# Kernel optimization log

Measured on AMD Instinct MI355X. Metric: run time of the kernel, lower is better.

Reference implementation:

```python
import jax, jax.numpy as jnp
import numpy as np

N = 4096        # batch size (rows)
K = 4           # instances per class -> num_instances in the torch code
D = 256         # embedding dim
MARGIN = 0.5
SAMPLE_KEY = jax.random.key(42)  # fixed key: deterministic stand-in for torch.multinomial


def setup_inputs() -> dict:
    key = jax.random.key(0)
    x = jax.random.normal(key, (N, D), dtype=jnp.float32)
    # L2-normalize like typical metric-learning embeddings so sims are in [-1, 1]
    inputs = x / jnp.linalg.norm(x, axis=1, keepdims=True)
    targets = (jnp.arange(N) // K).astype(jnp.int32)  # P*K batch: equal-size classes
    return {"inputs": inputs, "targets": targets}


def reference(inputs, targets):
    n = inputs.shape[0]
    km1 = K - 1                 # positives per row
    n_neg = n - K               # negatives per row

    sim = inputs @ inputs.T                                   # [n, n]
    same = targets[:, None] == targets[None, :]
    eye = jnp.eye(n, dtype=bool)
    pos_mask = same & ~eye
    neg_mask = ~same

    # masked_select + per-row sort: masked entries -> +inf, ascending sort,
    # keep first count entries (counts are uniform across rows)
    pos_sorted = jnp.sort(jnp.where(pos_mask, sim, jnp.inf), axis=1)[:, :km1]   # [n, K-1]
    neg_sorted = jnp.sort(jnp.where(neg_mask, sim, jnp.inf), axis=1)[:, :n_neg] # [n, n-K]

    pos_d = jnp.mean(pos_sorted)
    neg_d = jnp.mean(neg_sorted)

    # GaussDistribution per row over negatives
    neg_mean = jnp.mean(neg_sorted, axis=1, keepdims=True)
    neg_std = jnp.sqrt(jnp.mean((neg_sorted - neg_mean) ** 2, axis=1, keepdims=True))
    # NOTE: the original uses exp(+(x-mu)^2 / (2 sigma^2)) (no minus sign) -- faithful
    logprob = (neg_sorted - neg_mean) ** 2 / (2.0 * neg_std ** 2)               # [n, n-K]

    # multinomial without replacement ~ Gumbel top-k on log-weights
    gumbel = -jnp.log(-jnp.log(
        jax.random.uniform(SAMPLE_KEY, logprob.shape, minval=1e-20, maxval=1.0)))
    _, neg_idx = jax.lax.top_k(logprob + gumbel, km1)                            # [n, K-1]
    neg_pair = jnp.take_along_axis(neg_sorted, neg_idx, axis=1)                  # [n, K-1]

    pos_loss = jnp.mean(jnp.log1p(jnp.exp(-2.0 * (pos_sorted - MARGIN))), axis=1)
    neg_loss = 0.04 * jnp.mean(jnp.log1p(jnp.exp(50.0 * (neg_pair - MARGIN))), axis=1)
    loss = jnp.sum(pos_loss + neg_loss) / n

    # prec: fraction of rows where hardest positive > hardest sampled negative + 0.05
    c = jnp.sum(pos_sorted[:, -1] > jnp.max(neg_pair, axis=1) + 0.05)
    prec = c.astype(jnp.float32) / n

    return loss, prec, pos_d, neg_d
```

## Files before the change

kernel.cpp:

```cpp
#include <hip/hip_runtime.h>
#include <hip/hip_bf16.h>
#include <cstdint>
#include <cfloat>
#include <math.h>

#define NN 4096
#define DD 256
#define NNEG 4092
#define MARGIN 0.5f
#define NB 4096

__device__ __forceinline__ uint32_t rotl32(uint32_t x, int r) {
  return (x << r) | (x >> (32 - r));
}

__device__ __forceinline__ void threefry2x32_42(uint32_t x0, uint32_t x1,
                                                uint32_t& o0, uint32_t& o1) {
  const uint32_t k0 = 0u, k1 = 42u;
  const uint32_t k2 = k0 ^ k1 ^ 0x1BD11BDAu;
  x0 += k0; x1 += k1;
#define TF_R(r) { x0 += x1; x1 = rotl32(x1, r); x1 ^= x0; }
  TF_R(13) TF_R(15) TF_R(26) TF_R(6)
  x0 += k1; x1 += k2 + 1u;
  TF_R(17) TF_R(29) TF_R(16) TF_R(24)
  x0 += k2; x1 += k0 + 2u;
  TF_R(13) TF_R(15) TF_R(26) TF_R(6)
  x0 += k0; x1 += k1 + 3u;
  TF_R(17) TF_R(29) TF_R(16) TF_R(24)
  x0 += k1; x1 += k2 + 4u;
  TF_R(13) TF_R(15) TF_R(26) TF_R(6)
  x0 += k2; x1 += k0 + 5u;
#undef TF_R
  o0 = x0; o1 = x1;
}

__device__ __forceinline__ float gumbel_at(uint32_t f) {
  uint32_t o0, o1;
  threefry2x32_42(0u, f, o0, o1);
  uint32_t bits = o0 ^ o1;
  uint32_t fb = (bits >> 9) | 0x3F800000u;
  float fl = __uint_as_float(fb) - 1.0f;
  float u = fmaxf(1e-20f, fl + 1e-20f);
  return -logf(-logf(u));
}

__device__ __forceinline__ int bucket_of(float v) {
  return (int)fminf(fmaxf((v + 0.5f) * (float)NB, 0.0f), (float)(NB - 1));
}

#define BT 128
#define NT (NN / BT)
#define BK 64
#define LDSS 68

__global__ __launch_bounds__(256) void gemm_sim(const float* __restrict__ X,
                                                float* __restrict__ S) {
  __shared__ float As[BT * LDSS];
  __shared__ float Bs[BT * LDSS];
  const int tid = threadIdx.x;
  const int tx = tid & 15, ty = tid >> 4;

  int b = blockIdx.x, bi = 0;
  while (b >= NT - bi) { b -= NT - bi; bi++; }
  const int bj = bi + b;
  const int rowBase = bi * BT, colBase = bj * BT;

  float acc[8][8] = {};
  for (int kb = 0; kb < DD; kb += BK) {
#pragma unroll
    for (int it = 0; it < 8; ++it) {
      int idx = tid + 256 * it;
      int r = idx >> 4, c4 = idx & 15;
      float4 av = *(const float4*)(X + (size_t)(rowBase + r) * DD + kb + c4 * 4);
      float4 bv = *(const float4*)(X + (size_t)(colBase + r) * DD + kb + c4 * 4);
      *(float4*)(As + r * LDSS + c4 * 4) = av;
      *(float4*)(Bs + r * LDSS + c4 * 4) = bv;
    }
    __syncthreads();
    for (int k = 0; k < BK; k += 4) {
      float4 a[8], bfr[8];
#pragma unroll
      for (int i = 0; i < 8; ++i) a[i] = *(const float4*)(As + (ty + 16 * i) * LDSS + k);
#pragma unroll
      for (int j = 0; j < 8; ++j) bfr[j] = *(const float4*)(Bs + (tx + 16 * j) * LDSS + k);
#pragma unroll
      for (int i = 0; i < 8; ++i)
#pragma unroll
        for (int j = 0; j < 8; ++j) {
          acc[i][j] += a[i].x * bfr[j].x;
          acc[i][j] += a[i].y * bfr[j].y;
          acc[i][j] += a[i].z * bfr[j].z;
          acc[i][j] += a[i].w * bfr[j].w;
        }
    }
    __syncthreads();
  }
#pragma unroll
  for (int i = 0; i < 8; ++i)
#pragma unroll
    for (int j = 0; j < 8; ++j)
      S[(size_t)(rowBase + ty + 16 * i) * NN + colBase + tx + 16 * j] = acc[i][j];
  if (bi != bj) {
#pragma unroll
    for (int i = 0; i < 8; ++i)
#pragma unroll
      for (int j = 0; j < 8; ++j)
        S[(size_t)(colBase + tx + 16 * j) * NN + rowBase + ty + 16 * i] = acc[i][j];
  }
}

__global__ __launch_bounds__(256) void row_kernel(const float* __restrict__ S,
                                                  float* __restrict__ acc) {
  __shared__ uint32_t hist[NB];
  __shared__ uint32_t offs[NB];
  __shared__ float sval[NN];
  __shared__ float sh[24];
  __shared__ uint32_t wtot[4];

  const int row = blockIdx.x;
  const int tid = threadIdx.x;
  const int lane = tid & 63, wid = tid >> 6;

#pragma unroll
  for (int it = 0; it < 4; ++it)
    ((uint4*)hist)[tid + 256 * it] = make_uint4(0u, 0u, 0u, 0u);

  const float4* src = (const float4*)(S + (size_t)row * NN);
  const int pslot = row >> 2;
  float vv[16];
#pragma unroll
  for (int it = 0; it < 4; ++it) {
    int slot = tid + 256 * it;
    float4 t4 = src[slot];
    if (slot == pslot) {
      sh[16] = t4.x; sh[17] = t4.y; sh[18] = t4.z; sh[19] = t4.w;
      t4.x = INFINITY; t4.y = INFINITY; t4.z = INFINITY; t4.w = INFINITY;
    }
    vv[4 * it + 0] = t4.x; vv[4 * it + 1] = t4.y;
    vv[4 * it + 2] = t4.z; vv[4 * it + 3] = t4.w;
  }

  float s = 0.0f;
#pragma unroll
  for (int e = 0; e < 16; ++e) if (vv[e] < 1e30f) s += vv[e];
#pragma unroll
  for (int off = 32; off > 0; off >>= 1) s += __shfl_down(s, off, 64);
  if (lane == 0) sh[5 + wid] = s;
  __syncthreads();

#pragma unroll
  for (int e = 0; e < 16; ++e) atomicAdd(&hist[bucket_of(vv[e])], 1u);

  if (tid == 0) {
    int self = row & 3;
    float p[3]; int m = 0;
#pragma unroll
    for (int c = 0; c < 4; ++c)
      if (c != self) p[m++] = sh[16 + c];
    float t;
    if (p[0] > p[1]) { t = p[0]; p[0] = p[1]; p[1] = t; }
    if (p[1] > p[2]) { t = p[1]; p[1] = p[2]; p[2] = t; }
    if (p[0] > p[1]) { t = p[0]; p[0] = p[1]; p[1] = t; }
    sh[0] = p[0]; sh[1] = p[1]; sh[2] = p[2];
    float tot = sh[5] + sh[6] + sh[7] + sh[8];
    sh[9] = tot;
    sh[3] = tot / (float)NNEG;
  }
  __syncthreads();

  uint32_t h[16];
  uint32_t s16 = 0;
#pragma unroll
  for (int jj = 0; jj < 4; ++jj) {
    uint4 h4 = ((const uint4*)hist)[tid * 4 + jj];
    h[4 * jj + 0] = h4.x; h[4 * jj + 1] = h4.y;
    h[4 * jj + 2] = h4.z; h[4 * jj + 3] = h4.w;
    s16 += h4.x + h4.y + h4.z + h4.w;
  }
  uint32_t inc = s16;
#pragma unroll
  for (int off = 1; off < 64; off <<= 1) {
    uint32_t n = __shfl_up(inc, (unsigned)off, 64);
    if (lane >= off) inc += n;
  }
  if (lane == 63) wtot[wid] = inc;

  const float mu = sh[3];
  float q = 0.0f;
#pragma unroll
  for (int e = 0; e < 16; ++e)
    if (vv[e] < 1e30f) { float d = vv[e] - mu; q += d * d; }
#pragma unroll
  for (int off = 32; off > 0; off >>= 1) q += __shfl_down(q, off, 64);
  if (lane == 0) sh[10 + wid] = q;
  __syncthreads();

  uint32_t wbase = 0;
  for (int w = 0; w < wid; ++w) wbase += wtot[w];
  uint32_t run = wbase + inc - s16;
#pragma unroll
  for (int jj = 0; jj < 4; ++jj) {
    uint4 o4;
    o4.x = run; run += h[4 * jj + 0];
    o4.y = run; run += h[4 * jj + 1];
    o4.z = run; run += h[4 * jj + 2];
    o4.w = run; run += h[4 * jj + 3];
    ((uint4*)offs)[tid * 4 + jj] = o4;
  }
  if (tid == 0) {
    float var = (sh[10] + sh[11] + sh[12] + sh[13]) / (float)NNEG;
    float sd = sqrtf(var);
    sh[4] = 1.0f / (2.0f * sd * sd);
  }
  __syncthreads();

#pragma unroll
  for (int e = 0; e < 16; ++e) {
    uint32_t sl = atomicAdd(&offs[bucket_of(vv[e])], 1u);
    sval[sl] = vv[e];
  }
  __syncthreads();

  const float inv2s2 = sh[4];
  const uint32_t fbase = (uint32_t)row * (uint32_t)NNEG;
  float s0 = -FLT_MAX, s1 = -FLT_MAX, s2 = -FLT_MAX;
  float v0 = 0.0f, v1 = 0.0f, v2 = 0.0f;
#pragma unroll 1
  for (int it = 0; it < 16; ++it) {
    int sl = tid + 256 * it;
    float v = sval[sl];
    if (v < 1e30f) {
      int bk = bucket_of(v);
      uint32_t end = offs[bk];
      uint32_t st = end - hist[bk];
      int cnt = (int)st;
      for (uint32_t u = st; u < end; ++u) {
        float w = sval[u];
        cnt += (w < v || (w == v && (int)u < sl)) ? 1 : 0;
      }
      float d = v - mu;
      float sc = d * d * inv2s2 + gumbel_at(fbase + (uint32_t)cnt);
      if (sc > s2) {
        if (sc > s1) {
          s2 = s1; v2 = v1;
          if (sc > s0) { s1 = s0; v1 = v0; s0 = sc; v0 = v; }
          else         { s1 = sc; v1 = v; }
        } else { s2 = sc; v2 = v; }
      }
    }
  }
  __syncthreads();

  float* rs = sval;
  float* rv = sval + 768;
  rs[tid * 3 + 0] = s0; rv[tid * 3 + 0] = v0;
  rs[tid * 3 + 1] = s1; rv[tid * 3 + 1] = v1;
  rs[tid * 3 + 2] = s2; rv[tid * 3 + 2] = v2;
  __syncthreads();

  if (tid < 64) {
    float g0 = -FLT_MAX, g1 = -FLT_MAX, g2 = -FLT_MAX;
    float w0 = 0.0f, w1 = 0.0f, w2 = 0.0f;
    for (int blk = 0; blk < 4; ++blk) {
      int b0 = (tid + 64 * blk) * 3;
      for (int e = 0; e < 3; ++e) {
        float sc = rs[b0 + e], v = rv[b0 + e];
        if (sc > g2) {
          if (sc > g1) {
            g2 = g1; w2 = w1;
            if (sc > g0) { g1 = g0; w1 = w0; g0 = sc; w0 = v; }
            else         { g1 = sc; w1 = v; }
          } else { g2 = sc; w2 = v; }
        }
      }
    }
    rs[tid * 3 + 0] = g0; rv[tid * 3 + 0] = w0;
    rs[tid * 3 + 1] = g1; rv[tid * 3 + 1] = w1;
    rs[tid * 3 + 2] = g2; rv[tid * 3 + 2] = w2;
  }
  __syncthreads();

  if (tid == 0) {
    float g0 = -FLT_MAX, g1 = -FLT_MAX, g2 = -FLT_MAX;
    float w0 = 0.0f, w1 = 0.0f, w2 = 0.0f;
    for (int i = 0; i < 192; ++i) {
      float sc = rs[i], v = rv[i];
      if (sc > g2) {
        if (sc > g1) {
          g2 = g1; w2 = w1;
          if (sc > g0) { g1 = g0; w1 = w0; g0 = sc; w0 = v; }
          else         { g1 = sc; w1 = v; }
        } else { g2 = sc; w2 = v; }
      }
    }
    float negmax = fmaxf(w0, fmaxf(w1, w2));
    float neg_loss = 0.04f * (log1pf(expf(50.0f * (w0 - MARGIN))) +
                              log1pf(expf(50.0f * (w1 - MARGIN))) +
                              log1pf(expf(50.0f * (w2 - MARGIN)))) / 3.0f;
    float p0 = sh[0], p1 = sh[1], p2 = sh[2];
    float pos_loss = (log1pf(expf(-2.0f * (p0 - MARGIN))) +
                      log1pf(expf(-2.0f * (p1 - MARGIN))) +
                      log1pf(expf(-2.0f * (p2 - MARGIN)))) / 3.0f;
    atomicAdd(&acc[0], pos_loss + neg_loss);
    if (p2 > negmax + 0.05f) atomicAdd(&acc[1], 1.0f);
    atomicAdd(&acc[2], p0 + p1 + p2);
    atomicAdd(&acc[3], sh[9]);
  }
}

__global__ void finalize(const float* __restrict__ acc, float* out) {
  if (threadIdx.x == 0 && blockIdx.x == 0) {
    out[0] = acc[0] / 4096.0f;
    out[1] = acc[1] / 4096.0f;
    out[2] = acc[2] / (4096.0f * 3.0f);
    out[3] = acc[3] / (4096.0f * 4092.0f);
  }
}

extern "C" void kernel_launch(void* const* d_in, const int* in_sizes, int n_in,
                              void* d_out, int out_size, void* d_ws, size_t ws_size,
                              hipStream_t stream) {
  (void)in_sizes; (void)n_in; (void)out_size; (void)ws_size;
  const float* X = (const float*)d_in[0];
  float* S = (float*)d_ws;
  float* acc = (float*)((char*)d_ws + (size_t)NN * NN * 4);
  hipMemsetAsync(acc, 0, 4 * sizeof(float), stream);
  gemm_sim<<<NT * (NT + 1) / 2, 256, 0, stream>>>(X, S);
  row_kernel<<<NN, 256, 0, stream>>>(S, acc);
  finalize<<<1, 64, 0, stream>>>(acc, (float*)d_out);
}
```

Measured before the change: 422.9 us.

## Pack row histogram into 16-bit pairs, halve GEMM K-tile, shuffle-reduce top-3

```diff
diff --git a/kernel.cpp b/kernel.cpp
--- a/kernel.cpp
+++ b/kernel.cpp
@@ -8,7 +8,8 @@
 #define DD 256
 #define NNEG 4092
 #define MARGIN 0.5f
-#define NB 4096
+#define NB 3584
+#define NW (NB / 2)
 
 __device__ __forceinline__ uint32_t rotl32(uint32_t x, int r) {
   return (x << r) | (x >> (32 - r));
@@ -50,8 +51,8 @@
 
 #define BT 128
 #define NT (NN / BT)
-#define BK 64
-#define LDSS 68
+#define BK 32
+#define LDSS 36
 
 __global__ __launch_bounds__(256) void gemm_sim(const float* __restrict__ X,
                                                 float* __restrict__ S) {
@@ -68,9 +69,9 @@
   float acc[8][8] = {};
   for (int kb = 0; kb < DD; kb += BK) {
 #pragma unroll
-    for (int it = 0; it < 8; ++it) {
+    for (int it = 0; it < 4; ++it) {
       int idx = tid + 256 * it;
-      int r = idx >> 4, c4 = idx & 15;
+      int r = idx >> 3, c4 = idx & 7;
       float4 av = *(const float4*)(X + (size_t)(rowBase + r) * DD + kb + c4 * 4);
       float4 bv = *(const float4*)(X + (size_t)(colBase + r) * DD + kb + c4 * 4);
       *(float4*)(As + r * LDSS + c4 * 4) = av;
@@ -109,12 +110,21 @@
   }
 }
 
+#define INSERT3(sc, v)                                              \
+  if ((sc) > s2) {                                                  \
+    if ((sc) > s1) {                                                \
+      s2 = s1; v2 = v1;                                             \
+      if ((sc) > s0) { s1 = s0; v1 = v0; s0 = (sc); v0 = (v); }     \
+      else           { s1 = (sc); v1 = (v); }                       \
+    } else { s2 = (sc); v2 = (v); }                                 \
+  }
+
 __global__ __launch_bounds__(256) void row_kernel(const float* __restrict__ S,
                                                   float* __restrict__ acc) {
-  __shared__ uint32_t hist[NB];
-  __shared__ uint32_t offs[NB];
+  __shared__ uint32_t histw[NW];
+  __shared__ uint32_t offsw[NW];
   __shared__ float sval[NN];
-  __shared__ float sh[24];
+  __shared__ float sh[48];
   __shared__ uint32_t wtot[4];
 
   const int row = blockIdx.x;
@@ -122,8 +132,7 @@
   const int lane = tid & 63, wid = tid >> 6;
 
 #pragma unroll
-  for (int it = 0; it < 4; ++it)
-    ((uint4*)hist)[tid + 256 * it] = make_uint4(0u, 0u, 0u, 0u);
+  for (int i = 0; i < 7; ++i) histw[tid + 256 * i] = 0u;
 
   const float4* src = (const float4*)(S + (size_t)row * NN);
   const int pslot = row >> 2;
@@ -149,8 +158,10 @@
   __syncthreads();
 
 #pragma unroll
-  for (int e = 0; e < 16; ++e) atomicAdd(&hist[bucket_of(vv[e])], 1u);
-
+  for (int e = 0; e < 16; ++e) {
+    int b = bucket_of(vv[e]);
+    atomicAdd(&histw[b >> 1], 1u << ((b & 1) << 4));
+  }
   if (tid == 0) {
     int self = row & 3;
     float p[3]; int m = 0;
@@ -168,16 +179,14 @@
   }
   __syncthreads();
 
-  uint32_t h[16];
-  uint32_t s16 = 0;
-#pragma unroll
-  for (int jj = 0; jj < 4; ++jj) {
-    uint4 h4 = ((const uint4*)hist)[tid * 4 + jj];
-    h[4 * jj + 0] = h4.x; h[4 * jj + 1] = h4.y;
-    h[4 * jj + 2] = h4.z; h[4 * jj + 3] = h4.w;
-    s16 += h4.x + h4.y + h4.z + h4.w;
-  }
-  uint32_t inc = s16;
+  uint32_t hw[7];
+  uint32_t s14 = 0;
+#pragma unroll
+  for (int j = 0; j < 7; ++j) {
+    hw[j] = histw[7 * tid + j];
+    s14 += (hw[j] & 0xFFFFu) + (hw[j] >> 16);
+  }
+  uint32_t inc = s14;
 #pragma unroll
   for (int off = 1; off < 64; off <<= 1) {
     uint32_t n = __shfl_up(inc, (unsigned)off, 64);
@@ -197,15 +206,12 @@
 
   uint32_t wbase = 0;
   for (int w = 0; w < wid; ++w) wbase += wtot[w];
-  uint32_t run = wbase + inc - s16;
-#pragma unroll
-  for (int jj = 0; jj < 4; ++jj) {
-    uint4 o4;
-    o4.x = run; run += h[4 * jj + 0];
-    o4.y = run; run += h[4 * jj + 1];
-    o4.z = run; run += h[4 * jj + 2];
-    o4.w = run; run += h[4 * jj + 3];
-    ((uint4*)offs)[tid * 4 + jj] = o4;
+  uint32_t run = wbase + inc - s14;
+#pragma unroll
+  for (int j = 0; j < 7; ++j) {
+    uint32_t lo = run; run += hw[j] & 0xFFFFu;
+    uint32_t hi = run; run += hw[j] >> 16;
+    offsw[7 * tid + j] = lo | (hi << 16);
   }
   if (tid == 0) {
     float var = (sh[10] + sh[11] + sh[12] + sh[13]) / (float)NNEG;
@@ -216,7 +222,9 @@
 
 #pragma unroll
   for (int e = 0; e < 16; ++e) {
-    uint32_t sl = atomicAdd(&offs[bucket_of(vv[e])], 1u);
+    int b = bucket_of(vv[e]);
+    uint32_t old = atomicAdd(&offsw[b >> 1], 1u << ((b & 1) << 4));
+    uint32_t sl = (old >> ((b & 1) << 4)) & 0xFFFFu;
     sval[sl] = vv[e];
   }
   __syncthreads();
@@ -230,9 +238,11 @@
     int sl = tid + 256 * it;
     float v = sval[sl];
     if (v < 1e30f) {
-      int bk = bucket_of(v);
-      uint32_t end = offs[bk];
-      uint32_t st = end - hist[bk];
+      int b = bucket_of(v);
+      uint32_t sh16 = (uint32_t)((b & 1) << 4);
+      uint32_t end = (offsw[b >> 1] >> sh16) & 0xFFFFu;
+      uint32_t cntb = (histw[b >> 1] >> sh16) & 0xFFFFu;
+      uint32_t st = end - cntb;
       int cnt = (int)st;
       for (uint32_t u = st; u < end; ++u) {
         float w = sval[u];
@@ -240,58 +250,38 @@
       }
       float d = v - mu;
       float sc = d * d * inv2s2 + gumbel_at(fbase + (uint32_t)cnt);
-      if (sc > s2) {
-        if (sc > s1) {
-          s2 = s1; v2 = v1;
-          if (sc > s0) { s1 = s0; v1 = v0; s0 = sc; v0 = v; }
-          else         { s1 = sc; v1 = v; }
-        } else { s2 = sc; v2 = v; }
-      }
-    }
-  }
-  __syncthreads();
-
-  float* rs = sval;
-  float* rv = sval + 768;
-  rs[tid * 3 + 0] = s0; rv[tid * 3 + 0] = v0;
-  rs[tid * 3 + 1] = s1; rv[tid * 3 + 1] = v1;
-  rs[tid * 3 + 2] = s2; rv[tid * 3 + 2] = v2;
-  __syncthreads();
-
-  if (tid < 64) {
-    float g0 = -FLT_MAX, g1 = -FLT_MAX, g2 = -FLT_MAX;
-    float w0 = 0.0f, w1 = 0.0f, w2 = 0.0f;
-    for (int blk = 0; blk < 4; ++blk) {
-      int b0 = (tid + 64 * blk) * 3;
-      for (int e = 0; e < 3; ++e) {
-        float sc = rs[b0 + e], v = rv[b0 + e];
-        if (sc > g2) {
-          if (sc > g1) {
-            g2 = g1; w2 = w1;
-            if (sc > g0) { g1 = g0; w1 = w0; g0 = sc; w0 = v; }
-            else         { g1 = sc; w1 = v; }
-          } else { g2 = sc; w2 = v; }
-        }
-      }
-    }
-    rs[tid * 3 + 0] = g0; rv[tid * 3 + 0] = w0;
-    rs[tid * 3 + 1] = g1; rv[tid * 3 + 1] = w1;
-    rs[tid * 3 + 2] = g2; rv[tid * 3 + 2] = w2;
+      INSERT3(sc, v)
+    }
+  }
+
+#pragma unroll
+  for (int dlt = 1; dlt < 64; dlt <<= 1) {
+    float t0 = __shfl_xor(s0, dlt, 64), u0 = __shfl_xor(v0, dlt, 64);
+    float t1 = __shfl_xor(s1, dlt, 64), u1 = __shfl_xor(v1, dlt, 64);
+    float t2 = __shfl_xor(s2, dlt, 64), u2 = __shfl_xor(v2, dlt, 64);
+    INSERT3(t0, u0)
+    INSERT3(t1, u1)
+    INSERT3(t2, u2)
+  }
+  if (lane == 0) {
+    int b0 = 24 + wid * 6;
+    sh[b0 + 0] = s0; sh[b0 + 1] = v0;
+    sh[b0 + 2] = s1; sh[b0 + 3] = v1;
+    sh[b0 + 4] = s2; sh[b0 + 5] = v2;
   }
   __syncthreads();
 
   if (tid == 0) {
     float g0 = -FLT_MAX, g1 = -FLT_MAX, g2 = -FLT_MAX;
     float w0 = 0.0f, w1 = 0.0f, w2 = 0.0f;
-    for (int i = 0; i < 192; ++i) {
-      float sc = rs[i], v = rv[i];
-      if (sc > g2) {
-        if (sc > g1) {
-          g2 = g1; w2 = w1;
-          if (sc > g0) { g1 = g0; w1 = w0; g0 = sc; w0 = v; }
-          else         { g1 = sc; w1 = v; }
-        } else { g2 = sc; w2 = v; }
+    {
+      float s0 = g0, s1 = g1, s2 = g2, v0 = w0, v1 = w1, v2 = w2;
+#pragma unroll
+      for (int i = 0; i < 12; ++i) {
+        float sc = sh[24 + 2 * i], v = sh[24 + 2 * i + 1];
+        INSERT3(sc, v)
       }
+      g0 = s0; g1 = s1; g2 = s2; w0 = v0; w1 = v1; w2 = v2;
     }
     float negmax = fmaxf(w0, fmaxf(w1, w2));
     float neg_loss = 0.04f * (log1pf(expf(50.0f * (w0 - MARGIN))) +
```

New measurement: 368.2 us. 12.9% less time.
